# Kernel tuning notes

Measured on AMD Instinct MI355X. Metric: run time of the kernel, lower is better.

The kernel has to match this reference:

```python
import jax, jax.numpy as jnp
import numpy as np

B, L, DIM = 4, 9216, 256
NH, NP = 8, 4
HD = DIM // NH  # 32
SIDE = int(np.sqrt(L))  # 96


def setup_inputs() -> dict:
    key = jax.random.key(0)
    ks = jax.random.split(key, 8)
    s = 0.05
    return {
        "query": jax.random.normal(ks[0], (B, L, DIM), jnp.float32),
        "key": jax.random.normal(ks[1], (B, L, DIM), jnp.float32),
        "value": jax.random.normal(ks[2], (B, L, DIM), jnp.float32),
        "Wv": jax.random.normal(ks[3], (DIM, DIM), jnp.float32) * s,
        "bv": jnp.zeros((DIM,), jnp.float32),
        "Woff": jax.random.normal(ks[4], (DIM, NH * NP * 2), jnp.float32) * s,
        "boff": jnp.zeros((NH * NP * 2,), jnp.float32),
        "Wwt": jax.random.normal(ks[5], (DIM, NH * NP), jnp.float32) * s,
        "bwt": jnp.zeros((NH * NP,), jnp.float32),
        "Wo": jax.random.normal(ks[6], (DIM, DIM), jnp.float32) * s,
        "bo": jnp.zeros((DIM,), jnp.float32),
    }


def _deform_attn(query, value, Wv, bv, Woff, boff, Wwt, bwt, Wo, bo):
    Bq, Lq, D = query.shape
    h = w = SIDE
    # value projection -> [B, nH, L, hd]
    v = (value @ Wv + bv).reshape(Bq, Lq, NH, HD).transpose(0, 2, 1, 3)
    # reference points in [0,1]: ref[...,0]=x (varies fast), ref[...,1]=y (row-major flatten)
    ys = jnp.linspace(0.0, 1.0, h)
    xs = jnp.linspace(0.0, 1.0, w)
    y_ref = jnp.repeat(ys, w)  # [L]
    x_ref = jnp.tile(xs, h)    # [L]
    ref = jnp.stack([x_ref, y_ref], axis=-1)  # [L, 2]
    # offsets [B, nH, Lq, NP, 2] and softmax weights [B, nH, Lq, NP]
    offset = (query @ Woff + boff).reshape(Bq, Lq, NH, NP, 2).transpose(0, 2, 1, 3, 4)
    wt = jax.nn.softmax(
        (query @ Wwt + bwt).reshape(Bq, Lq, NH, NP).transpose(0, 2, 1, 3), axis=-1
    )
    loc = jnp.clip(ref[None, None, :, None, :] + offset, 0.0, 1.0)
    # faithful to source: component 0 scales by (h-1) -> row, component 1 by (w-1) -> col
    rows = loc[..., 0] * (h - 1)  # [B, nH, Lq, NP]
    cols = loc[..., 1] * (w - 1)
    r0 = jnp.floor(rows)
    c0 = jnp.floor(cols)
    fr = (rows - r0)[..., None]  # [B, nH, Lq, NP, 1]
    fc = (cols - c0)[..., None]
    r0i = r0.astype(jnp.int32)
    c0i = c0.astype(jnp.int32)
    r1i = jnp.minimum(r0i + 1, h - 1)
    c1i = jnp.minimum(c0i + 1, w - 1)

    def gather(ri, ci):
        idx = (ri * w + ci).reshape(Bq, NH, Lq * NP)
        g = jnp.take_along_axis(v, idx[..., None], axis=2)  # [B, nH, Lq*NP, hd]
        return g.reshape(Bq, NH, Lq, NP, HD)

    samp = (
        gather(r0i, c0i) * (1.0 - fr) * (1.0 - fc)
        + gather(r0i, c1i) * (1.0 - fr) * fc
        + gather(r1i, c0i) * fr * (1.0 - fc)
        + gather(r1i, c1i) * fr * fc
    )  # [B, nH, Lq, NP, hd]
    out = jnp.einsum("bhqp,bhqpd->bhqd", wt, samp)
    out = out.transpose(0, 2, 1, 3).reshape(Bq, Lq, D)
    return out @ Wo + bo


def reference(query, key, value, Wv, bv, Woff, boff, Wwt, bwt, Wo, bo):
    # key never influences the output in the source module (k is computed but unused)
    return _deform_attn(query, value, Wv, bv, Woff, boff, Wwt, bwt, Wo, bo)
```

## Files before the change

kernel.cpp:

```cpp
#include <hip/hip_runtime.h>
#include <hip/hip_bf16.h>

#define Bq   4
#define Lq   9216
#define DIMc 256
#define NHc  8
#define NPc  4
#define HDc  32
#define SIDEc 96

using f32x4  = __attribute__((ext_vector_type(4))) float;
using bf16x8 = __attribute__((ext_vector_type(8))) short;
using u16x8  = __attribute__((ext_vector_type(8))) unsigned short;
using h16x4  = __attribute__((ext_vector_type(4))) _Float16;

static __device__ __forceinline__ short f2bf(float x) {
    union { __hip_bfloat16 h; short s; } u;
    u.h = __float2bfloat16(x);
    return u.s;
}
static __device__ __forceinline__ float bfbits(unsigned short s) {
    union { unsigned u; float f; } v; v.u = ((unsigned)s) << 16; return v.f;
}

__global__ void prep(const float* __restrict__ Wv, const float* __restrict__ Wo,
                     const float* __restrict__ Woff, const float* __restrict__ Wwt,
                     short* __restrict__ WvT, short* __restrict__ WoT,
                     short* __restrict__ WpHi, short* __restrict__ WpLo) {
    const int id = blockIdx.x, t = threadIdx.x;
    if (id < 64) {
        __shared__ float tile[256][8];
        const float* W = (id < 32) ? Wv : Wo;
        short* T = (id < 32) ? WvT : WoT;
        const int n0 = (id & 31) * 8;
        const float4 a = *(const float4*)&W[t * 256 + n0];
        const float4 b = *(const float4*)&W[t * 256 + n0 + 4];
        tile[t][0] = a.x; tile[t][1] = a.y; tile[t][2] = a.z; tile[t][3] = a.w;
        tile[t][4] = b.x; tile[t][5] = b.y; tile[t][6] = b.z; tile[t][7] = b.w;
        __syncthreads();
        const int n = n0 + (t >> 5), kk = (t & 31) * 8;
        bf16x8 v;
#pragma unroll
        for (int e = 0; e < 8; ++e) v[e] = f2bf(tile[kk + e][t >> 5]);
        *(bf16x8*)&T[n * 256 + kk] = v;
    } else {
        const int p = id - 64;
        const float x = (p < 64) ? Woff[t * 64 + p] : Wwt[t * 32 + (p - 64)];
        const short h = f2bf(x);
        WpHi[p * 256 + t] = h;
        WpLo[p * 256 + t] = f2bf(x - bfbits((unsigned short)h));
    }
}

template<bool VOUT, bool BF16IN>
__global__ __launch_bounds__(256, 3) void gemm_mfma(
        const float* __restrict__ Xf, const short* Xb,
        const short* __restrict__ WT, const float* __restrict__ bias,
        __hip_bfloat16* __restrict__ Yv, float* Yo) {
    __shared__ short As[64][264];
    const int t = threadIdx.x;
    const int base = blockIdx.x * 64;

    if (BF16IN) {
#pragma unroll
        for (int p = 0; p < 8; ++p) {
            const int c = p * 256 + t;
            const int r = c >> 5, k0 = (c & 31) * 8;
            *(bf16x8*)&As[r][k0] = *(const bf16x8*)&Xb[((long)blockIdx.x << 15) + r * 256 + k0];
        }
    } else {
        const float4* X4 = (const float4*)(Xf + (long)base * DIMc);
#pragma unroll
        for (int p = 0; p < 8; ++p) {
            const int c = p * 256 + t;
            const int r = c >> 5, kq = (c & 31) * 2;
            const float4 a = X4[r * 64 + kq];
            const float4 b = X4[r * 64 + kq + 1];
            bf16x8 v;
            v[0] = f2bf(a.x); v[1] = f2bf(a.y); v[2] = f2bf(a.z); v[3] = f2bf(a.w);
            v[4] = f2bf(b.x); v[5] = f2bf(b.y); v[6] = f2bf(b.z); v[7] = f2bf(b.w);
            *(bf16x8*)&As[r][kq * 4] = v;
        }
    }
    __syncthreads();

    const int lane = t & 63, wc = t >> 6;
    const int lr = lane & 15, lq = lane >> 4;

    f32x4 acc[4][4];
#pragma unroll
    for (int i = 0; i < 4; ++i)
#pragma unroll
        for (int j = 0; j < 4; ++j) acc[i][j] = (f32x4){0.f, 0.f, 0.f, 0.f};

#pragma unroll
    for (int ks = 0; ks < 8; ++ks) {
        const int k0 = ks * 32 + lq * 8;
        bf16x8 a[4], b[4];
#pragma unroll
        for (int i = 0; i < 4; ++i)
            a[i] = *(const bf16x8*)&As[i * 16 + lr][k0];
#pragma unroll
        for (int j = 0; j < 4; ++j)
            b[j] = *(const bf16x8*)&WT[(wc * 64 + j * 16 + lr) * 256 + k0];
#pragma unroll
        for (int i = 0; i < 4; ++i)
#pragma unroll
            for (int j = 0; j < 4; ++j)
                acc[i][j] = __builtin_amdgcn_mfma_f32_16x16x32_bf16(a[i], b[j], acc[i][j], 0, 0, 0);
    }

    const int b_ = base / Lq;
    const int l0 = base % Lq;
#pragma unroll
    for (int i = 0; i < 4; ++i) {
        const int mrow = i * 16 + lq * 4;
#pragma unroll
        for (int j = 0; j < 4; ++j) {
            const int n  = wc * 64 + j * 16 + lr;
            const float bb = bias[n];
            const f32x4 v = acc[i][j];
            if (VOUT) {
                const int h = n >> 5, d = n & 31;
                __hip_bfloat16* yb = Yv + (((long)(b_ * NHc + h)) * Lq + (l0 + mrow)) * HDc + d;
#pragma unroll
                for (int reg = 0; reg < 4; ++reg)
                    yb[(long)reg * HDc] = __float2bfloat16(v[reg] + bb);
            } else {
                float* yo = Yo + (long)(base + mrow) * DIMc + n;
#pragma unroll
                for (int reg = 0; reg < 4; ++reg)
                    yo[(long)reg * DIMc] = v[reg] + bb;
            }
        }
    }
}

__global__ __launch_bounds__(256, 3) void deform_fused3(
        const float* __restrict__ Q,
        const short* __restrict__ WpHi, const short* __restrict__ WpLo,
        const float* __restrict__ boff, const float* __restrict__ bwt,
        const __hip_bfloat16* __restrict__ vws,
        __hip_bfloat16* __restrict__ midb) {
    __shared__ float prjs[32 * 96];
    __shared__ int   recI[1024];
    __shared__ h16x4 recW[1024];

    const int t = threadIdx.x;
    const int bid = (int)blockIdx.x;
    const int lb = (bid & 7) * 144 + (bid >> 3);
    const int base = lb * 32;
    const int b  = base / Lq;
    const int l0 = base % Lq;

    const int lane = t & 63, w = t >> 6;
    const int lr = lane & 15, lq = lane >> 4;

    {
        const int rt = w >> 1, cg = w & 1;
        f32x4 pacc[3];
#pragma unroll
        for (int jj = 0; jj < 3; ++jj) pacc[jj] = (f32x4){0.f, 0.f, 0.f, 0.f};
        const float* Qrow = Q + (long)(base + rt * 16 + lr) * DIMc;
#pragma unroll
        for (int ks = 0; ks < 8; ++ks) {
            const int k0 = ks * 32 + lq * 8;
            const float4 a0 = *(const float4*)(Qrow + k0);
            const float4 a1 = *(const float4*)(Qrow + k0 + 4);
            const float xs[8] = {a0.x, a0.y, a0.z, a0.w, a1.x, a1.y, a1.z, a1.w};
            bf16x8 ah, al;
#pragma unroll
            for (int e = 0; e < 8; ++e) {
                const short hh = f2bf(xs[e]);
                ah[e] = hh;
                al[e] = f2bf(xs[e] - bfbits((unsigned short)hh));
            }
#pragma unroll
            for (int jj = 0; jj < 3; ++jj) {
                const int c = cg * 48 + jj * 16 + lr;
                const bf16x8 bh = *(const bf16x8*)&WpHi[c * 256 + k0];
                const bf16x8 bl = *(const bf16x8*)&WpLo[c * 256 + k0];
                pacc[jj] = __builtin_amdgcn_mfma_f32_16x16x32_bf16(ah, bh, pacc[jj], 0, 0, 0);
                pacc[jj] = __builtin_amdgcn_mfma_f32_16x16x32_bf16(ah, bl, pacc[jj], 0, 0, 0);
                pacc[jj] = __builtin_amdgcn_mfma_f32_16x16x32_bf16(al, bh, pacc[jj], 0, 0, 0);
            }
        }
#pragma unroll
        for (int jj = 0; jj < 3; ++jj) {
            const int col = cg * 48 + jj * 16 + lr;
            const float bb = (col < 64) ? boff[col] : bwt[col - 64];
#pragma unroll
            for (int reg = 0; reg < 4; ++reg) {
                const int row = rt * 16 + lq * 4 + reg;
                prjs[row * 96 + col] = pacc[jj][reg] + bb;
            }
        }
    }
    __syncthreads();

#pragma unroll
    for (int i = 0; i < 4; ++i) {
        const int s = i * 256 + t;
        const int r = s >> 5, u = s & 31;
        const int h = u >> 2, p = u & 3;
        const int l = l0 + r;
        const float* pr = &prjs[r * 96];
        const float inv = 1.0f / (SIDEc - 1);
        const float xr = (float)(l % SIDEc) * inv;
        const float yr = (float)(l / SIDEc) * inv;

        const float4 lg = *(const float4*)&pr[64 + h * 4];
        const float m = fmaxf(fmaxf(lg.x, lg.y), fmaxf(lg.z, lg.w));
        const float e0 = expf(lg.x - m), e1 = expf(lg.y - m);
        const float e2 = expf(lg.z - m), e3 = expf(lg.w - m);
        const float sum = e0 + e1 + e2 + e3;
        const float ep = (p == 0) ? e0 : (p == 1) ? e1 : (p == 2) ? e2 : e3;
        const float wt = ep / sum;

        const float lx = fminf(fmaxf(xr + pr[u * 2 + 0], 0.f), 1.f);
        const float ly = fminf(fmaxf(yr + pr[u * 2 + 1], 0.f), 1.f);
        const float rowf = lx * (float)(SIDEc - 1);
        const float colf = ly * (float)(SIDEc - 1);
        const float r0f = floorf(rowf), c0f = floorf(colf);
        const int r0 = (int)r0f, c0 = (int)c0f;
        const float fr = rowf - r0f, fc = colf - c0f;
        const int drow = (r0 < SIDEc - 1) ? 1 : 0;
        const int dcol = (c0 < SIDEc - 1) ? 1 : 0;
        recI[s] = (r0 * SIDEc + c0) | (drow << 16) | (dcol << 17);
        h16x4 wh;
        wh[0] = (_Float16)(wt * (1.f - fr) * (1.f - fc));
        wh[1] = (_Float16)(wt * (1.f - fr) * fc);
        wh[2] = (_Float16)(wt * fr * (1.f - fc));
        wh[3] = (_Float16)(wt * fr * fc);
        recW[s] = wh;
    }
    __syncthreads();

    const int h = (t >> 2) & 7, dq = t & 3;
    const int rhalf = (t >> 5) & 1, wid = t >> 6;
    const __hip_bfloat16* vb = vws + ((long)(b * NHc + h) * Lq) * HDc + dq * 8;
    const int chan = (t & 31) * 8;

#pragma unroll
    for (int pass = 0; pass < 4; ++pass) {
        const int r = pass * 8 + wid * 2 + rhalf;
        float acc[8];
#pragma unroll
        for (int e = 0; e < 8; ++e) acc[e] = 0.f;
#pragma unroll
        for (int p = 0; p < 4; ++p) {
            const int   mt = recI[r * 32 + h * 4 + p];
            const h16x4 wh = recW[r * 32 + h * 4 + p];
            const float w0 = (float)wh[0], w1 = (float)wh[1];
            const float w2 = (float)wh[2], w3 = (float)wh[3];
            const int sl = mt & 0xFFFF;
            const int dr = (mt & 0x10000) ? SIDEc * HDc : 0;
            const int dc = (mt & 0x20000) ? HDc : 0;
            const __hip_bfloat16* pv = vb + (long)sl * HDc;
            const u16x8 u00 = *(const u16x8*)(pv);
            const u16x8 u01 = *(const u16x8*)(pv + dc);
            const u16x8 u10 = *(const u16x8*)(pv + dr);
            const u16x8 u11 = *(const u16x8*)(pv + dr + dc);
#pragma unroll
            for (int e = 0; e < 8; ++e)
                acc[e] += w0 * bfbits(u00[e]) + w1 * bfbits(u01[e])
                        + w2 * bfbits(u10[e]) + w3 * bfbits(u11[e]);
        }
        const int rg = base + r;
        u16x8 o;
#pragma unroll
        for (int e = 0; e < 8; ++e) o[e] = (unsigned short)f2bf(acc[e]);
        *(u16x8*)(midb + ((long)(rg >> 6) << 15) + ((rg & 63) << 8) + chan) = o;
    }
}

extern "C" void kernel_launch(void* const* d_in, const int* in_sizes, int n_in,
                              void* d_out, int out_size, void* d_ws, size_t ws_size,
                              hipStream_t stream) {
    const float* query = (const float*)d_in[0];
    const float* value = (const float*)d_in[2];
    const float* Wv    = (const float*)d_in[3];
    const float* bv    = (const float*)d_in[4];
    const float* Woff  = (const float*)d_in[5];
    const float* boff  = (const float*)d_in[6];
    const float* Wwt   = (const float*)d_in[7];
    const float* bwt   = (const float*)d_in[8];
    const float* Wo    = (const float*)d_in[9];
    const float* bo    = (const float*)d_in[10];

    float* out = (float*)d_out;
    char*  ws  = (char*)d_ws;
    __hip_bfloat16* vws = (__hip_bfloat16*)ws;
    short* WvT  = (short*)(ws + 18874368);
    short* WoT  = (short*)(ws + 18874368 + 131072);
    short* WpHi = (short*)(ws + 18874368 + 262144);
    short* WpLo = (short*)(ws + 18874368 + 262144 + 49152);
    __hip_bfloat16* midb = (__hip_bfloat16*)d_out;

    const int nrows = Bq * Lq;

    prep<<<160, 256, 0, stream>>>(Wv, Wo, Woff, Wwt, WvT, WoT, WpHi, WpLo);
    gemm_mfma<true, false><<<nrows / 64, 256, 0, stream>>>(value, nullptr, WvT, bv, vws, nullptr);
    deform_fused3<<<nrows / 32, 256, 0, stream>>>(query, WpHi, WpLo, boff, bwt, vws, midb);
    gemm_mfma<false, true><<<nrows / 64, 256, 0, stream>>>(nullptr, (const short*)midb, WoT, bo, nullptr, out);
}
```

Baseline: 104.8 us.

## Use 384-thread blocks in fused deform kernel with one column tile per wave

The fused projection/sampling kernel now runs 384 threads (6 waves) per 32-row block. In the projection stage each wave owns one 16-column tile across both 16-row halves, so each weight fragment is reused for two MFMA chains. The sampling and gather stages are redistributed over 384 threads with guarded loops, which leaves some threads idle in the last pass. The launch bound now asks for 6 blocks per CU, which raises the number of waves in flight to hide gather latency but may limit registers per thread.

```diff
diff --git a/kernel.cpp b/kernel.cpp
--- a/kernel.cpp
+++ b/kernel.cpp
@@ -136,7 +136,7 @@
     }
 }
 
-__global__ __launch_bounds__(256, 3) void deform_fused3(
+__global__ __launch_bounds__(384, 6) void deform_fused4(
         const float* __restrict__ Q,
         const short* __restrict__ WpHi, const short* __restrict__ WpLo,
         const float* __restrict__ boff, const float* __restrict__ bwt,
@@ -157,120 +157,120 @@
     const int lr = lane & 15, lq = lane >> 4;
 
     {
-        const int rt = w >> 1, cg = w & 1;
-        f32x4 pacc[3];
-#pragma unroll
-        for (int jj = 0; jj < 3; ++jj) pacc[jj] = (f32x4){0.f, 0.f, 0.f, 0.f};
-        const float* Qrow = Q + (long)(base + rt * 16 + lr) * DIMc;
+        f32x4 p0 = (f32x4){0.f,0.f,0.f,0.f}, p1 = (f32x4){0.f,0.f,0.f,0.f};
+        const float* Qr0 = Q + (long)(base + lr) * DIMc;
+        const float* Qr1 = Q + (long)(base + 16 + lr) * DIMc;
+        const int col = w * 16 + lr;
 #pragma unroll
         for (int ks = 0; ks < 8; ++ks) {
             const int k0 = ks * 32 + lq * 8;
-            const float4 a0 = *(const float4*)(Qrow + k0);
-            const float4 a1 = *(const float4*)(Qrow + k0 + 4);
-            const float xs[8] = {a0.x, a0.y, a0.z, a0.w, a1.x, a1.y, a1.z, a1.w};
-            bf16x8 ah, al;
+            const float4 a0 = *(const float4*)(Qr0 + k0);
+            const float4 a1 = *(const float4*)(Qr0 + k0 + 4);
+            const float4 c0 = *(const float4*)(Qr1 + k0);
+            const float4 c1 = *(const float4*)(Qr1 + k0 + 4);
+            const float x0[8] = {a0.x, a0.y, a0.z, a0.w, a1.x, a1.y, a1.z, a1.w};
+            const float x1[8] = {c0.x, c0.y, c0.z, c0.w, c1.x, c1.y, c1.z, c1.w};
+            bf16x8 ah0, al0, ah1, al1;
 #pragma unroll
             for (int e = 0; e < 8; ++e) {
-                const short hh = f2bf(xs[e]);
-                ah[e] = hh;
-                al[e] = f2bf(xs[e] - bfbits((unsigned short)hh));
+                short hh = f2bf(x0[e]);
+                ah0[e] = hh; al0[e] = f2bf(x0[e] - bfbits((unsigned short)hh));
+                hh = f2bf(x1[e]);
+                ah1[e] = hh; al1[e] = f2bf(x1[e] - bfbits((unsigned short)hh));
             }
-#pragma unroll
-            for (int jj = 0; jj < 3; ++jj) {
-                const int c = cg * 48 + jj * 16 + lr;
-                const bf16x8 bh = *(const bf16x8*)&WpHi[c * 256 + k0];
-                const bf16x8 bl = *(const bf16x8*)&WpLo[c * 256 + k0];
-                pacc[jj] = __builtin_amdgcn_mfma_f32_16x16x32_bf16(ah, bh, pacc[jj], 0, 0, 0);
-                pacc[jj] = __builtin_amdgcn_mfma_f32_16x16x32_bf16(ah, bl, pacc[jj], 0, 0, 0);
-                pacc[jj] = __builtin_amdgcn_mfma_f32_16x16x32_bf16(al, bh, pacc[jj], 0, 0, 0);
+            const bf16x8 bh = *(const bf16x8*)&WpHi[col * 256 + k0];
+            const bf16x8 bl = *(const bf16x8*)&WpLo[col * 256 + k0];
+            p0 = __builtin_amdgcn_mfma_f32_16x16x32_bf16(ah0, bh, p0, 0, 0, 0);
+            p0 = __builtin_amdgcn_mfma_f32_16x16x32_bf16(ah0, bl, p0, 0, 0, 0);
+            p0 = __builtin_amdgcn_mfma_f32_16x16x32_bf16(al0, bh, p0, 0, 0, 0);
+            p1 = __builtin_amdgcn_mfma_f32_16x16x32_bf16(ah1, bh, p1, 0, 0, 0);
+            p1 = __builtin_amdgcn_mfma_f32_16x16x32_bf16(ah1, bl, p1, 0, 0, 0);
+            p1 = __builtin_amdgcn_mfma_f32_16x16x32_bf16(al1, bh, p1, 0, 0, 0);
+        }
+        const float bb = (col < 64) ? boff[col] : bwt[col - 64];
+#pragma unroll
+        for (int reg = 0; reg < 4; ++reg) {
+            prjs[(lq * 4 + reg) * 96 + col]        = p0[reg] + bb;
+            prjs[(16 + lq * 4 + reg) * 96 + col]   = p1[reg] + bb;
+        }
+    }
+    __syncthreads();
+
+#pragma unroll
+    for (int i = 0; i < 3; ++i) {
+        const int s = i * 384 + t;
+        if (s < 1024) {
+            const int r = s >> 5, u = s & 31;
+            const int h = u >> 2, p = u & 3;
+            const int l = l0 + r;
+            const float* pr = &prjs[r * 96];
+            const float inv = 1.0f / (SIDEc - 1);
+            const float xr = (float)(l % SIDEc) * inv;
+            const float yr = (float)(l / SIDEc) * inv;
+
+            const float4 lg = *(const float4*)&pr[64 + h * 4];
+            const float m = fmaxf(fmaxf(lg.x, lg.y), fmaxf(lg.z, lg.w));
+            const float e0 = expf(lg.x - m), e1 = expf(lg.y - m);
+            const float e2 = expf(lg.z - m), e3 = expf(lg.w - m);
+            const float sum = e0 + e1 + e2 + e3;
+            const float ep = (p == 0) ? e0 : (p == 1) ? e1 : (p == 2) ? e2 : e3;
+            const float wt = ep / sum;
+
+            const float lx = fminf(fmaxf(xr + pr[u * 2 + 0], 0.f), 1.f);
+            const float ly = fminf(fmaxf(yr + pr[u * 2 + 1], 0.f), 1.f);
+            const float rowf = lx * (float)(SIDEc - 1);
+            const float colf = ly * (float)(SIDEc - 1);
+            const float r0f = floorf(rowf), c0f = floorf(colf);
+            const int r0 = (int)r0f, c0 = (int)c0f;
+            const float fr = rowf - r0f, fc = colf - c0f;
+            const int drow = (r0 < SIDEc - 1) ? 1 : 0;
+            const int dcol = (c0 < SIDEc - 1) ? 1 : 0;
+            recI[s] = (r0 * SIDEc + c0) | (drow << 16) | (dcol << 17);
+            h16x4 wh;
+            wh[0] = (_Float16)(wt * (1.f - fr) * (1.f - fc));
+            wh[1] = (_Float16)(wt * (1.f - fr) * fc);
+            wh[2] = (_Float16)(wt * fr * (1.f - fc));
+            wh[3] = (_Float16)(wt * fr * fc);
+            recW[s] = wh;
+        }
+    }
+    __syncthreads();
+
+#pragma unroll
+    for (int pass = 0; pass < 3; ++pass) {
+        const int s = pass * 384 + t;
+        if (s < 1024) {
+            const int r = s >> 5, u = s & 31;
+            const int h = u >> 2, dq = u & 3;
+            const __hip_bfloat16* vb = vws + ((long)(b * NHc + h) * Lq) * HDc + dq * 8;
+            float acc[8];
+#pragma unroll
+            for (int e = 0; e < 8; ++e) acc[e] = 0.f;
+#pragma unroll
+            for (int p = 0; p < 4; ++p) {
+                const int   mt = recI[r * 32 + h * 4 + p];
+                const h16x4 wh = recW[r * 32 + h * 4 + p];
+                const float w0 = (float)wh[0], w1 = (float)wh[1];
+                const float w2 = (float)wh[2], w3 = (float)wh[3];
+                const int sl = mt & 0xFFFF;
+                const int dr = (mt & 0x10000) ? SIDEc * HDc : 0;
+                const int dc = (mt & 0x20000) ? HDc : 0;
+                const __hip_bfloat16* pv = vb + (long)sl * HDc;
+                const u16x8 u00 = *(const u16x8*)(pv);
+                const u16x8 u01 = *(const u16x8*)(pv + dc);
+                const u16x8 u10 = *(const u16x8*)(pv + dr);
+                const u16x8 u11 = *(const u16x8*)(pv + dr + dc);
+#pragma unroll
+                for (int e = 0; e < 8; ++e)
+                    acc[e] += w0 * bfbits(u00[e]) + w1 * bfbits(u01[e])
+                            + w2 * bfbits(u10[e]) + w3 * bfbits(u11[e]);
             }
-        }
-#pragma unroll
-        for (int jj = 0; jj < 3; ++jj) {
-            const int col = cg * 48 + jj * 16 + lr;
-            const float bb = (col < 64) ? boff[col] : bwt[col - 64];
-#pragma unroll
-            for (int reg = 0; reg < 4; ++reg) {
-                const int row = rt * 16 + lq * 4 + reg;
-                prjs[row * 96 + col] = pacc[jj][reg] + bb;
-            }
-        }
-    }
-    __syncthreads();
-
-#pragma unroll
-    for (int i = 0; i < 4; ++i) {
-        const int s = i * 256 + t;
-        const int r = s >> 5, u = s & 31;
-        const int h = u >> 2, p = u & 3;
-        const int l = l0 + r;
-        const float* pr = &prjs[r * 96];
-        const float inv = 1.0f / (SIDEc - 1);
-        const float xr = (float)(l % SIDEc) * inv;
-        const float yr = (float)(l / SIDEc) * inv;
-
-        const float4 lg = *(const float4*)&pr[64 + h * 4];
-        const float m = fmaxf(fmaxf(lg.x, lg.y), fmaxf(lg.z, lg.w));
-        const float e0 = expf(lg.x - m), e1 = expf(lg.y - m);
-        const float e2 = expf(lg.z - m), e3 = expf(lg.w - m);
-        const float sum = e0 + e1 + e2 + e3;
-        const float ep = (p == 0) ? e0 : (p == 1) ? e1 : (p == 2) ? e2 : e3;
-        const float wt = ep / sum;
-
-        const float lx = fminf(fmaxf(xr + pr[u * 2 + 0], 0.f), 1.f);
-        const float ly = fminf(fmaxf(yr + pr[u * 2 + 1], 0.f), 1.f);
-        const float rowf = lx * (float)(SIDEc - 1);
-        const float colf = ly * (float)(SIDEc - 1);
-        const float r0f = floorf(rowf), c0f = floorf(colf);
-        const int r0 = (int)r0f, c0 = (int)c0f;
-        const float fr = rowf - r0f, fc = colf - c0f;
-        const int drow = (r0 < SIDEc - 1) ? 1 : 0;
-        const int dcol = (c0 < SIDEc - 1) ? 1 : 0;
-        recI[s] = (r0 * SIDEc + c0) | (drow << 16) | (dcol << 17);
-        h16x4 wh;
-        wh[0] = (_Float16)(wt * (1.f - fr) * (1.f - fc));
-        wh[1] = (_Float16)(wt * (1.f - fr) * fc);
-        wh[2] = (_Float16)(wt * fr * (1.f - fc));
-        wh[3] = (_Float16)(wt * fr * fc);
-        recW[s] = wh;
-    }
-    __syncthreads();
-
-    const int h = (t >> 2) & 7, dq = t & 3;
-    const int rhalf = (t >> 5) & 1, wid = t >> 6;
-    const __hip_bfloat16* vb = vws + ((long)(b * NHc + h) * Lq) * HDc + dq * 8;
-    const int chan = (t & 31) * 8;
-
-#pragma unroll
-    for (int pass = 0; pass < 4; ++pass) {
-        const int r = pass * 8 + wid * 2 + rhalf;
-        float acc[8];
-#pragma unroll
-        for (int e = 0; e < 8; ++e) acc[e] = 0.f;
-#pragma unroll
-        for (int p = 0; p < 4; ++p) {
-            const int   mt = recI[r * 32 + h * 4 + p];
-            const h16x4 wh = recW[r * 32 + h * 4 + p];
-            const float w0 = (float)wh[0], w1 = (float)wh[1];
-            const float w2 = (float)wh[2], w3 = (float)wh[3];
-            const int sl = mt & 0xFFFF;
-            const int dr = (mt & 0x10000) ? SIDEc * HDc : 0;
-            const int dc = (mt & 0x20000) ? HDc : 0;
-            const __hip_bfloat16* pv = vb + (long)sl * HDc;
-            const u16x8 u00 = *(const u16x8*)(pv);
-            const u16x8 u01 = *(const u16x8*)(pv + dc);
-            const u16x8 u10 = *(const u16x8*)(pv + dr);
-            const u16x8 u11 = *(const u16x8*)(pv + dr + dc);
-#pragma unroll
-            for (int e = 0; e < 8; ++e)
-                acc[e] += w0 * bfbits(u00[e]) + w1 * bfbits(u01[e])
-                        + w2 * bfbits(u10[e]) + w3 * bfbits(u11[e]);
-        }
-        const int rg = base + r;
-        u16x8 o;
-#pragma unroll
-        for (int e = 0; e < 8; ++e) o[e] = (unsigned short)f2bf(acc[e]);
-        *(u16x8*)(midb + ((long)(rg >> 6) << 15) + ((rg & 63) << 8) + chan) = o;
+            const int rg = base + r;
+            u16x8 o;
+#pragma unroll
+            for (int e = 0; e < 8; ++e) o[e] = (unsigned short)f2bf(acc[e]);
+            *(u16x8*)(midb + ((long)(rg >> 6) << 15) + ((rg & 63) << 8) + u * 8) = o;
+        }
     }
 }
 
@@ -301,6 +301,6 @@
 
     prep<<<160, 256, 0, stream>>>(Wv, Wo, Woff, Wwt, WvT, WoT, WpHi, WpLo);
     gemm_mfma<true, false><<<nrows / 64, 256, 0, stream>>>(value, nullptr, WvT, bv, vws, nullptr);
-    deform_fused3<<<nrows / 32, 256, 0, stream>>>(query, WpHi, WpLo, boff, bwt, vws, midb);
+    deform_fused4<<<nrows / 32, 384, 0, stream>>>(query, WpHi, WpLo, boff, bwt, vws, midb);
     gemm_mfma<false, true><<<nrows / 64, 256, 0, stream>>>(nullptr, (const short*)midb, WoT, bo, nullptr, out);
 }
```

New measurement: 209.1 us. 99.5% more time.

## Halve rows per block in fused deform kernel and redistribute projection MFMA work

Applied to the files above, without the earlier changes.

The fused offset/weight projection and sampling kernel now handles 16 query rows per block instead of 32, which doubles the grid to 2304 blocks and halves shared memory use. The projection GEMM is re-split so each of the four waves computes one or two 16-column tiles over a single 16-row tile, with waves 0-1 also taking the last two column tiles. Sampling is reindexed so each thread handles one row/head/quarter-chunk per pass over two passes. The aim is more parallelism and occupancy. The cost is weight reloads per block for the projection and some imbalance between waves in the MFMA phase.

```diff
diff --git a/kernel.cpp b/kernel.cpp
--- a/kernel.cpp
+++ b/kernel.cpp
@@ -136,20 +136,20 @@
     }
 }
 
-__global__ __launch_bounds__(256, 3) void deform_fused3(
+__global__ __launch_bounds__(256, 3) void deform_fused5(
         const float* __restrict__ Q,
         const short* __restrict__ WpHi, const short* __restrict__ WpLo,
         const float* __restrict__ boff, const float* __restrict__ bwt,
         const __hip_bfloat16* __restrict__ vws,
         __hip_bfloat16* __restrict__ midb) {
-    __shared__ float prjs[32 * 96];
-    __shared__ int   recI[1024];
-    __shared__ h16x4 recW[1024];
+    __shared__ float prjs[16 * 96];
+    __shared__ int   recI[512];
+    __shared__ h16x4 recW[512];
 
     const int t = threadIdx.x;
     const int bid = (int)blockIdx.x;
-    const int lb = (bid & 7) * 144 + (bid >> 3);
-    const int base = lb * 32;
+    const int lb = (bid & 7) * 288 + (bid >> 3);
+    const int base = lb * 16;
     const int b  = base / Lq;
     const int l0 = base % Lq;
 
@@ -157,11 +157,10 @@
     const int lr = lane & 15, lq = lane >> 4;
 
     {
-        const int rt = w >> 1, cg = w & 1;
-        f32x4 pacc[3];
-#pragma unroll
-        for (int jj = 0; jj < 3; ++jj) pacc[jj] = (f32x4){0.f, 0.f, 0.f, 0.f};
-        const float* Qrow = Q + (long)(base + rt * 16 + lr) * DIMc;
+        f32x4 pa0 = (f32x4){0.f,0.f,0.f,0.f}, pa1 = (f32x4){0.f,0.f,0.f,0.f};
+        const float* Qrow = Q + (long)(base + lr) * DIMc;
+        const int col0 = w * 16 + lr;
+        const int col1 = (4 + w) * 16 + lr;
 #pragma unroll
         for (int ks = 0; ks < 8; ++ks) {
             const int k0 = ks * 32 + lq * 8;
@@ -175,31 +174,36 @@
                 ah[e] = hh;
                 al[e] = f2bf(xs[e] - bfbits((unsigned short)hh));
             }
-#pragma unroll
-            for (int jj = 0; jj < 3; ++jj) {
-                const int c = cg * 48 + jj * 16 + lr;
-                const bf16x8 bh = *(const bf16x8*)&WpHi[c * 256 + k0];
-                const bf16x8 bl = *(const bf16x8*)&WpLo[c * 256 + k0];
-                pacc[jj] = __builtin_amdgcn_mfma_f32_16x16x32_bf16(ah, bh, pacc[jj], 0, 0, 0);
-                pacc[jj] = __builtin_amdgcn_mfma_f32_16x16x32_bf16(ah, bl, pacc[jj], 0, 0, 0);
-                pacc[jj] = __builtin_amdgcn_mfma_f32_16x16x32_bf16(al, bh, pacc[jj], 0, 0, 0);
+            {
+                const bf16x8 bh = *(const bf16x8*)&WpHi[col0 * 256 + k0];
+                const bf16x8 bl = *(const bf16x8*)&WpLo[col0 * 256 + k0];
+                pa0 = __builtin_amdgcn_mfma_f32_16x16x32_bf16(ah, bh, pa0, 0, 0, 0);
+                pa0 = __builtin_amdgcn_mfma_f32_16x16x32_bf16(ah, bl, pa0, 0, 0, 0);
+                pa0 = __builtin_amdgcn_mfma_f32_16x16x32_bf16(al, bh, pa0, 0, 0, 0);
             }
-        }
-#pragma unroll
-        for (int jj = 0; jj < 3; ++jj) {
-            const int col = cg * 48 + jj * 16 + lr;
-            const float bb = (col < 64) ? boff[col] : bwt[col - 64];
-#pragma unroll
-            for (int reg = 0; reg < 4; ++reg) {
-                const int row = rt * 16 + lq * 4 + reg;
-                prjs[row * 96 + col] = pacc[jj][reg] + bb;
+            if (w < 2) {
+                const bf16x8 bh = *(const bf16x8*)&WpHi[col1 * 256 + k0];
+                const bf16x8 bl = *(const bf16x8*)&WpLo[col1 * 256 + k0];
+                pa1 = __builtin_amdgcn_mfma_f32_16x16x32_bf16(ah, bh, pa1, 0, 0, 0);
+                pa1 = __builtin_amdgcn_mfma_f32_16x16x32_bf16(ah, bl, pa1, 0, 0, 0);
+                pa1 = __builtin_amdgcn_mfma_f32_16x16x32_bf16(al, bh, pa1, 0, 0, 0);
             }
         }
+        const float bb0 = (col0 < 64) ? boff[col0] : bwt[col0 - 64];
+#pragma unroll
+        for (int reg = 0; reg < 4; ++reg)
+            prjs[(lq * 4 + reg) * 96 + col0] = pa0[reg] + bb0;
+        if (w < 2) {
+            const float bb1 = (col1 < 64) ? boff[col1] : bwt[col1 - 64];
+#pragma unroll
+            for (int reg = 0; reg < 4; ++reg)
+                prjs[(lq * 4 + reg) * 96 + col1] = pa1[reg] + bb1;
+        }
     }
     __syncthreads();
 
 #pragma unroll
-    for (int i = 0; i < 4; ++i) {
+    for (int i = 0; i < 2; ++i) {
         const int s = i * 256 + t;
         const int r = s >> 5, u = s & 31;
         const int h = u >> 2, p = u & 3;
@@ -236,14 +240,12 @@
     }
     __syncthreads();
 
-    const int h = (t >> 2) & 7, dq = t & 3;
-    const int rhalf = (t >> 5) & 1, wid = t >> 6;
-    const __hip_bfloat16* vb = vws + ((long)(b * NHc + h) * Lq) * HDc + dq * 8;
-    const int chan = (t & 31) * 8;
-
-#pragma unroll
-    for (int pass = 0; pass < 4; ++pass) {
-        const int r = pass * 8 + wid * 2 + rhalf;
+#pragma unroll
+    for (int pass = 0; pass < 2; ++pass) {
+        const int s = pass * 256 + t;
+        const int r = s >> 5, u = s & 31;
+        const int h = u >> 2, dq = u & 3;
+        const __hip_bfloat16* vb = vws + ((long)(b * NHc + h) * Lq) * HDc + dq * 8;
         float acc[8];
 #pragma unroll
         for (int e = 0; e < 8; ++e) acc[e] = 0.f;
@@ -270,7 +272,7 @@
         u16x8 o;
 #pragma unroll
         for (int e = 0; e < 8; ++e) o[e] = (unsigned short)f2bf(acc[e]);
-        *(u16x8*)(midb + ((long)(rg >> 6) << 15) + ((rg & 63) << 8) + chan) = o;
+        *(u16x8*)(midb + ((long)(rg >> 6) << 15) + ((rg & 63) << 8) + u * 8) = o;
     }
 }
 
@@ -301,6 +303,6 @@
 
     prep<<<160, 256, 0, stream>>>(Wv, Wo, Woff, Wwt, WvT, WoT, WpHi, WpLo);
     gemm_mfma<true, false><<<nrows / 64, 256, 0, stream>>>(value, nullptr, WvT, bv, vws, nullptr);
-    deform_fused3<<<nrows / 32, 256, 0, stream>>>(query, WpHi, WpLo, boff, bwt, vws, midb);
+    deform_fused5<<<nrows / 16, 256, 0, stream>>>(query, WpHi, WpLo, boff, bwt, vws, midb);
     gemm_mfma<false, true><<<nrows / 64, 256, 0, stream>>>(nullptr, (const short*)midb, WoT, bo, nullptr, out);
 }
```

New measurement: 113.4 us. 8.2% more time.
